# Kernel tuning notes

Hardware: AMD Instinct MI355X
Metric: run time of the kernel (lower is better)

## Reference

```python
import jax, jax.numpy as jnp
import numpy as np

FG_THR = 0.7
BG_THR = 0.3
NUM_PER_IMAGE = 256
NUM_POS_MAX = int(NUM_PER_IMAGE * 0.5)  # positive_ratio = 0.5
BBOX_W = (1.0, 1.0, 1.0, 1.0)
BETA = 1.0 / 9.0


def _permute(t, C):
    # N x (A*C) x H x W -> N x (H*W*A) x C, matching RPNLoss.permute
    N, _, H, W = t.shape
    t = t.reshape(N, -1, C, H, W)
    t = jnp.transpose(t, (0, 3, 4, 1, 2))
    return t.reshape(N, -1, C)


def _iou(a, b):
    # a: [N,4], b: [M,4] -> [N,M] (with +1 box convention, as in source)
    x_tl = jnp.maximum(a[:, None, 0], b[None, :, 0])
    y_tl = jnp.maximum(a[:, None, 1], b[None, :, 1])
    x_rb = jnp.minimum(a[:, None, 2], b[None, :, 2])
    y_rb = jnp.minimum(a[:, None, 3], b[None, :, 3])
    inter = jnp.clip(x_rb - x_tl + 1.0, 0.0) * jnp.clip(y_rb - y_tl + 1.0, 0.0)
    area1 = (a[:, 2] - a[:, 0] + 1.0) * (a[:, 3] - a[:, 1] + 1.0)
    area2 = (b[:, 2] - b[:, 0] + 1.0) * (b[:, 3] - b[:, 1] + 1.0)
    return inter / (area1[:, None] + area2[None, :] - inter)


def _encode(anchors, targets):
    ws = anchors[:, 2] - anchors[:, 0] + 1.0
    hs = anchors[:, 3] - anchors[:, 1] + 1.0
    x_ctr = anchors[:, 0] + 0.5 * ws
    y_ctr = anchors[:, 1] + 0.5 * hs
    t_ws = targets[:, 2] - targets[:, 0] + 1.0
    t_hs = targets[:, 3] - targets[:, 1] + 1.0
    t_x = targets[:, 0] + 0.5 * t_ws
    t_y = targets[:, 1] + 0.5 * t_hs
    wx, wy, ww, wh = BBOX_W
    tx = wx * (t_x - x_ctr) / ws
    ty = wy * (t_y - y_ctr) / hs
    tw = ww * jnp.log(t_ws / ws)
    th = wh * jnp.log(t_hs / hs)
    return jnp.stack([tx, ty, tw, th], axis=1)


def _bce_logits(l, t):
    return jnp.maximum(l, 0.0) - l * t + jnp.log1p(jnp.exp(-jnp.abs(l)))


def _per_image(anchor, logit, breg, size, target, key):
    N = anchor.shape[0]
    ious = _iou(anchor, target)  # [N, M]
    vals = ious.max(axis=1)
    ori = jnp.argmax(ious, axis=1).astype(jnp.int32)
    inds = jnp.where(vals < BG_THR, -1, ori)
    inds = jnp.where((vals >= BG_THR) & (vals < FG_THR), -2, inds)
    # low-quality matches: anchors achieving the per-target max IoU keep their argmax
    col_max = ious.max(axis=0)
    restore = (ious == col_max[None, :]).any(axis=1)
    inds = jnp.where(restore, ori, inds)
    # filter_anchors: keep anchors fully inside the image (size = (h, w))
    inside = (anchor[:, 0] >= 0) & (anchor[:, 1] >= 0) & \
             (anchor[:, 2] <= size[1] - 1.0) & (anchor[:, 3] <= size[0] - 1.0)
    inds = jnp.where(inside, inds, -2)

    pos = inds >= 0
    neg = inds == -1
    # random sampling via random priorities + fixed-size top_k with validity masks
    r = jax.random.uniform(key, (N,))
    pos_vals, pos_idx = jax.lax.top_k(jnp.where(pos, r, -1.0), NUM_POS_MAX)
    valid_pos = pos_vals >= 0.0
    num_pos = valid_pos.sum()
    neg_vals, neg_idx = jax.lax.top_k(jnp.where(neg, r, -1.0), NUM_PER_IMAGE)
    valid_neg = (neg_vals >= 0.0) & (jnp.arange(NUM_PER_IMAGE) < (NUM_PER_IMAGE - num_pos))

    # classification loss terms (BCE with logits); pos target 1, neg target 0
    vp = valid_pos.astype(logit.dtype)
    vn = valid_neg.astype(logit.dtype)
    cls_sum = jnp.sum(_bce_logits(logit[pos_idx], 1.0) * vp) + \
              jnp.sum(_bce_logits(logit[neg_idx], 0.0) * vn)
    count = num_pos + valid_neg.sum()

    m = jnp.clip(inds[pos_idx], 0, None)
    offsets = _encode(anchor[pos_idx], target[m])
    diff = jnp.abs(breg[pos_idx] - offsets)
    sl1 = jnp.where(diff < BETA, 0.5 * diff * diff / BETA, diff - 0.5 * BETA)
    reg_sum = jnp.sum(sl1 * vp[:, None])
    return cls_sum, count, reg_sum


def reference(anchors, logits, bbox_regs, sizes, targets):
    B = anchors.shape[0]
    log = _permute(logits, 1)[..., 0]      # [B, H*W*A]
    breg = _permute(bbox_regs, 4)          # [B, H*W*A, 4]
    keys = jax.random.split(jax.random.key(42), B)
    cls_s, cnt, reg_s = jax.vmap(_per_image)(anchors, log, breg, sizes, targets, keys)
    total = jnp.sum(cnt).astype(anchors.dtype)
    cls_loss = jnp.sum(cls_s) / total
    reg_loss = jnp.sum(reg_s) / total
    return jnp.stack([cls_loss, reg_loss])


def setup_inputs() -> dict:
    key = jax.random.key(0)
    ks = jax.random.split(key, 10)
    B, A, H, W, M = 4, 3, 168, 256, 32
    N = H * W * A
    IMG_H, IMG_W = 800.0, 1333.0
    x1 = jax.random.uniform(ks[0], (B, N)) * 1200.0
    y1 = jax.random.uniform(ks[1], (B, N)) * 700.0
    aw = jax.random.uniform(ks[2], (B, N)) * 300.0 + 16.0
    ah = jax.random.uniform(ks[3], (B, N)) * 300.0 + 16.0
    anchors = jnp.stack([x1, y1, x1 + aw, y1 + ah], axis=-1)  # some out of image -> filtered
    tx1 = jax.random.uniform(ks[4], (B, M)) * 1000.0
    ty1 = jax.random.uniform(ks[5], (B, M)) * 500.0
    tw = jax.random.uniform(ks[6], (B, M)) * 250.0 + 30.0
    th = jax.random.uniform(ks[7], (B, M)) * 200.0 + 30.0
    targets = jnp.stack([tx1, ty1, jnp.minimum(tx1 + tw, IMG_W - 1.0),
                         jnp.minimum(ty1 + th, IMG_H - 1.0)], axis=-1)
    logits = jax.random.normal(ks[8], (B, A, H, W), dtype=jnp.float32)
    bbox_regs = jax.random.normal(ks[9], (B, 4 * A, H, W), dtype=jnp.float32) * 0.1
    sizes = jnp.tile(jnp.array([IMG_H, IMG_W], dtype=jnp.float32), (B, 1))
    return {"anchors": anchors, "logits": logits, "bbox_regs": bbox_regs,
            "sizes": sizes, "targets": targets}
```

## Files before the change

### kernel.cpp

```cpp
#include <hip/hip_runtime.h>
#include <stdint.h>

#define Bn 4
#define An 3
#define Hn 168
#define Wn 256
#define Mn 32
#define HWn (Hn*Wn)
#define Nn (HWn*An)
#define POS_CAP 8192
#define NPERIM 256
#define NPOSMAX 128
#define FG_THR 0.7f
#define BG_THR 0.3f
#define BETA (1.0f/9.0f)

#define NBLK 126
#define APT 4
#define STRIDE (NBLK * 256)
#define NWAVES (NBLK * 4)
#define BUCKET_CAP 256
#define TSEG_CAP 256

#define OFF_POSCNT 0
#define OFF_COUNT  8
#define OFF_CLS    9
#define OFF_REG    10
#define OFF_DONE   11
#define OFF_BINCNT 16
#define OFF_BINBCE 4112
#define ZERO_WORDS 8208
#define OFF_WPCM   8208
#define OFF_TSEGC  72720
#define OFF_PLIST  74736
#define OFF_BUCKET 140272
#define OFF_TSEG   2237424

__device__ __forceinline__ uint32_t rotl32(uint32_t v, int n) { return (v << n) | (v >> (32 - n)); }

__device__ __forceinline__ void tf2x32(uint32_t k0, uint32_t k1, uint32_t x0, uint32_t x1,
                                       uint32_t& o0, uint32_t& o1) {
    uint32_t k2 = k0 ^ k1 ^ 0x1BD11BDAu;
    x0 += k0; x1 += k1;
    x0 += x1; x1 = rotl32(x1, 13); x1 ^= x0;
    x0 += x1; x1 = rotl32(x1, 15); x1 ^= x0;
    x0 += x1; x1 = rotl32(x1, 26); x1 ^= x0;
    x0 += x1; x1 = rotl32(x1, 6);  x1 ^= x0;
    x0 += k1; x1 += k2 + 1u;
    x0 += x1; x1 = rotl32(x1, 17); x1 ^= x0;
    x0 += x1; x1 = rotl32(x1, 29); x1 ^= x0;
    x0 += x1; x1 = rotl32(x1, 16); x1 ^= x0;
    x0 += x1; x1 = rotl32(x1, 24); x1 ^= x0;
    x0 += k2; x1 += k0 + 2u;
    x0 += x1; x1 = rotl32(x1, 13); x1 ^= x0;
    x0 += x1; x1 = rotl32(x1, 15); x1 ^= x0;
    x0 += x1; x1 = rotl32(x1, 26); x1 ^= x0;
    x0 += x1; x1 = rotl32(x1, 6);  x1 ^= x0;
    x0 += k0; x1 += k1 + 3u;
    x0 += x1; x1 = rotl32(x1, 17); x1 ^= x0;
    x0 += x1; x1 = rotl32(x1, 29); x1 ^= x0;
    x0 += x1; x1 = rotl32(x1, 16); x1 ^= x0;
    x0 += x1; x1 = rotl32(x1, 24); x1 ^= x0;
    x0 += k1; x1 += k2 + 4u;
    x0 += x1; x1 = rotl32(x1, 13); x1 ^= x0;
    x0 += x1; x1 = rotl32(x1, 15); x1 ^= x0;
    x0 += x1; x1 = rotl32(x1, 26); x1 ^= x0;
    x0 += x1; x1 = rotl32(x1, 6);  x1 ^= x0;
    x0 += k2; x1 += k0 + 5u;
    o0 = x0; o1 = x1;
}

__device__ __forceinline__ uint32_t rng_m23(uint32_t k0, uint32_t k1, uint32_t i) {
    uint32_t o0, o1;
    tf2x32(k0, k1, 0u, i, o0, o1);
    return (o0 ^ o1) >> 9;
}

__device__ __forceinline__ uint32_t vload(const uint32_t* p) {
    return *(const volatile uint32_t*)p;
}

__device__ __forceinline__ float iou_one(float a0, float a1, float a2, float a3,
                                         float t0, float t1, float t2, float t3) {
    float xtl = fmaxf(a0, t0), ytl = fmaxf(a1, t1);
    float xrb = fminf(a2, t2), yrb = fminf(a3, t3);
    float iw = fmaxf(xrb - xtl + 1.0f, 0.0f);
    float ih = fmaxf(yrb - ytl + 1.0f, 0.0f);
    float inter = iw * ih;
    float area1 = (a2 - a0 + 1.0f) * (a3 - a1 + 1.0f);
    float area2 = (t2 - t0 + 1.0f) * (t3 - t1 + 1.0f);
    return inter * __builtin_amdgcn_rcpf(area1 + area2 - inter);
}

__device__ __forceinline__ float bce0(float l) {
    return fmaxf(l, 0.0f) + log1pf(expf(-fabsf(l)));
}

__device__ __forceinline__ bool sel_less(uint2 a, uint2 b) {
    return (a.x > b.x) || (a.x == b.x && a.y < b.y);
}

__device__ void bitonic_sort_shared(uint2* buf, int n) {
    for (int k = 2; k <= n; k <<= 1) {
        for (int j = k >> 1; j > 0; j >>= 1) {
            for (int t = (int)threadIdx.x; t < n; t += (int)blockDim.x) {
                int ixj = t ^ j;
                if (ixj > t) {
                    uint2 x = buf[t], y = buf[ixj];
                    bool up = ((t & k) == 0);
                    bool sw = up ? sel_less(y, x) : sel_less(x, y);
                    if (sw) { buf[t] = y; buf[ixj] = x; }
                }
            }
            __syncthreads();
        }
    }
}

__global__ void __launch_bounds__(256) k0_init(uint32_t* __restrict__ ws) {
    int i = blockIdx.x * 256 + (int)threadIdx.x;
    if (i < ZERO_WORDS) ws[i] = 0u;
}

__global__ void __launch_bounds__(256) k1_iou(const float* __restrict__ anchors,
                                              const float* __restrict__ targets,
                                              const float* __restrict__ sizes,
                                              const float* __restrict__ logits,
                                              uint32_t* __restrict__ ws) {
    const int b = blockIdx.y, j = blockIdx.x, tid = threadIdx.x;
    const int wid = tid >> 6, lane = tid & 63;

    uint32_t key0, key1;
    tf2x32(0u, 42u, 0u, (uint32_t)b, key0, key1);

    const int base = j * 256 + tid;
    float4 av[APT];
    #pragma unroll
    for (int k = 0; k < APT; ++k)
        av[k] = ((const float4*)anchors)[b * Nn + base + k * STRIDE];

    float rowmax[APT]; int ori[APT]; uint32_t tie[APT];
    #pragma unroll
    for (int k = 0; k < APT; ++k) { rowmax[k] = -1.0f; ori[k] = 0; tie[k] = 0u; }

    float mycm = 0.0f;
    #pragma unroll 4
    for (int t = 0; t < Mn; ++t) {
        float4 tv = ((const float4*)targets)[b * Mn + t];
        float io[APT];
        float m0 = 0.0f;
        #pragma unroll
        for (int k = 0; k < APT; ++k) {
            io[k] = iou_one(av[k].x, av[k].y, av[k].z, av[k].w, tv.x, tv.y, tv.z, tv.w);
            if (io[k] > rowmax[k]) { rowmax[k] = io[k]; ori[k] = t; }
            m0 = fmaxf(m0, io[k]);
        }
        #pragma unroll
        for (int o = 32; o > 0; o >>= 1) m0 = fmaxf(m0, __shfl_xor(m0, o, 64));
        if (lane == t) mycm = m0;
        #pragma unroll
        for (int k = 0; k < APT; ++k)
            tie[k] |= (io[k] == m0) ? (1u << t) : 0u;
    }

    const int wimg = j * 4 + wid;
    if (lane < Mn)
        ws[OFF_WPCM + ((size_t)b * NWAVES + wimg) * 32 + lane] = __float_as_uint(mycm);

    const float sh = sizes[b * 2 + 0], sw = sizes[b * 2 + 1];
    unsigned long long lt_mask = (lane == 63) ? 0x7FFFFFFFFFFFFFFFull
                                              : ((1ull << lane) - 1ull);
    uint4* tseg = (uint4*)(ws + OFF_TSEG) + ((size_t)b * NWAVES + wimg) * TSEG_CAP;
    uint32_t wcnt = 0;
    #pragma unroll
    for (int k = 0; k < APT; ++k) {
        const int i = base + k * STRIDE;
        bool inside = (av[k].x >= 0.0f) && (av[k].y >= 0.0f) &&
                      (av[k].z <= sw - 1.0f) && (av[k].w <= sh - 1.0f);
        bool fg = rowmax[k] >= FG_THR;
        bool bg = rowmax[k] < BG_THR;
        bool posn   = inside && fg;
        bool defern = inside && !fg && (tie[k] != 0u);
        bool negn   = inside && bg && (tie[k] == 0u);
        uint32_t m = rng_m23(key0, key1, (uint32_t)i);

        unsigned long long pmask = __ballot(posn);
        if (pmask) {
            int leader = __ffsll((long long)pmask) - 1;
            uint32_t bb = 0;
            if (lane == leader) bb = atomicAdd(&ws[OFF_POSCNT + b], (uint32_t)__popcll(pmask));
            bb = __shfl(bb, leader, 64);
            if (posn) {
                uint32_t p = bb + (uint32_t)__popcll(pmask & lt_mask);
                if (p < POS_CAP)
                    ((uint2*)(ws + OFF_PLIST))[(size_t)b * POS_CAP + p] =
                        make_uint2(m, (uint32_t)i | ((uint32_t)ori[k] << 17));
            }
        }
        unsigned long long dmask = __ballot(defern);
        if (defern) {
            uint32_t slot = wcnt + (uint32_t)__popcll(dmask & lt_mask);
            tseg[slot] = make_uint4(tie[k], m,
                                    (uint32_t)i | ((uint32_t)ori[k] << 17) | (bg ? (1u << 22) : 0u),
                                    0u);
        }
        wcnt += (uint32_t)__popcll(dmask);
        if (negn) {
            int bin = (int)(m >> 13);
            uint32_t slot = atomicAdd(&ws[OFF_BINCNT + (b << 10) + bin], 1u);
            if (slot < BUCKET_CAP)
                ((uint2*)(ws + OFF_BUCKET))[((((size_t)b << 10) + bin) << 8) + slot] =
                    make_uint2(m, (uint32_t)i);
            int a = i % An, hw = i / An;
            float l = logits[(b * An + a) * HWn + hw];
            atomicAdd((float*)&ws[OFF_BINBCE + (b << 10) + bin], bce0(l));
        }
    }
    if (lane == 0) ws[OFF_TSEGC + b * NWAVES + wimg] = wcnt;
}

__global__ void __launch_bounds__(1024) k3_final(const float* __restrict__ anchors,
                                                 const float* __restrict__ targets,
                                                 const float* __restrict__ logits,
                                                 const float* __restrict__ bregs,
                                                 uint32_t* __restrict__ ws,
                                                 float* __restrict__ out) {
    const int b = blockIdx.x, tid = threadIdx.x;
    __shared__ uint32_t cmbits[Mn];
    __shared__ float fred[1024];
    __shared__ uint32_t eq[512];
    __shared__ uint32_t incl[512];
    __shared__ uint32_t csum[1024];
    __shared__ uint2 buf[2048];
    __shared__ int s_bd, s_need;
    float cls = 0.0f, reg = 0.0f;

    {
        int t = tid & 31, sub = tid >> 5;
        float acc = 0.0f;
        for (int w = sub; w < NWAVES; w += 32)
            acc = fmaxf(acc, __uint_as_float(ws[OFF_WPCM + ((size_t)b * NWAVES + w) * 32 + t]));
        fred[tid] = acc;
        __syncthreads();
        if (sub == 0) {
            #pragma unroll
            for (int q = 1; q < 32; ++q) acc = fmaxf(acc, fred[t + 32 * q]);
            cmbits[t] = __float_as_uint(acc);
        }
    }
    __syncthreads();

    if (tid < NWAVES) {
        const uint32_t* wp = ws + OFF_WPCM + ((size_t)b * NWAVES + tid) * 32;
        uint32_t e = 0;
        #pragma unroll 8
        for (int t2 = 0; t2 < Mn; ++t2)
            e |= (wp[t2] == cmbits[t2]) ? (1u << t2) : 0u;
        eq[tid] = e;
    }
    if (tid < 512) incl[tid] = (tid < NWAVES) ? ws[OFF_TSEGC + b * NWAVES + tid] : 0u;
    __syncthreads();
    for (int off = 1; off < 512; off <<= 1) {
        uint32_t v = 0;
        if (tid < 512) { v = incl[tid]; if (tid >= off) v += incl[tid - off]; }
        __syncthreads();
        if (tid < 512) incl[tid] = v;
        __syncthreads();
    }
    const int ttotal = (int)incl[511];

    for (int f = tid; f < ttotal; f += 1024) {
        int lo = 0, hi = 511;
        while (lo < hi) { int mid = (lo + hi) >> 1; if ((int)incl[mid] > f) hi = mid; else lo = mid + 1; }
        const int w = lo;
        const int o = f - ((w > 0) ? (int)incl[w - 1] : 0);
        uint4 e = ((const uint4*)(ws + OFF_TSEG))[((size_t)b * NWAVES + w) * TSEG_CAP + o];
        int i = (int)(e.z & 0x1FFFFu);
        if (e.x & eq[w]) {
            uint32_t p = atomicAdd(&ws[OFF_POSCNT + b], 1u);
            if (p < POS_CAP)
                ((uint2*)(ws + OFF_PLIST))[(size_t)b * POS_CAP + p] =
                    make_uint2(e.y, e.z & 0x3FFFFFu);
        } else if (e.z & (1u << 22)) {
            uint32_t m = e.y;
            int bin = (int)(m >> 13);
            uint32_t slot = atomicAdd(&ws[OFF_BINCNT + (b << 10) + bin], 1u);
            if (slot < BUCKET_CAP)
                ((uint2*)(ws + OFF_BUCKET))[((((size_t)b << 10) + bin) << 8) + slot] =
                    make_uint2(m, (uint32_t)i);
            int a = i % An, hw = i / An;
            float l = logits[(b * An + a) * HWn + hw];
            atomicAdd((float*)&ws[OFF_BINBCE + (b << 10) + bin], bce0(l));
        }
    }
    __syncthreads();

    csum[tid] = vload(ws + OFF_BINCNT + (b << 10) + tid);
    __syncthreads();
    for (int off = 1; off < 1024; off <<= 1) {
        uint32_t v = csum[tid];
        uint32_t add = (tid + off < 1024) ? csum[tid + off] : 0u;
        __syncthreads();
        csum[tid] = v + add;
        __syncthreads();
    }
    uint32_t pc = vload(ws + OFF_POSCNT + b);
    int num_pos = (pc < (uint32_t)NPOSMAX) ? (int)pc : NPOSMAX;
    int k_neg = NPERIM - num_pos;
    uint32_t total = csum[0];
    if (tid == 0 && (int)total < k_neg) { s_bd = -1; s_need = 0; }
    {
        uint32_t inclv = csum[tid];
        uint32_t nxt = (tid < 1023) ? csum[tid + 1] : 0u;
        if ((int)total >= k_neg && (int)inclv >= k_neg && (int)nxt < k_neg) {
            s_bd = tid; s_need = k_neg - (int)nxt;
        }
    }
    if (tid == 0) {
        int sel_negs = ((int)total < k_neg) ? (int)total : k_neg;
        atomicAdd(&ws[OFF_COUNT], (uint32_t)(num_pos + sel_negs));
    }
    __syncthreads();
    const int bd = s_bd, need = s_need;
    if ((int)tid > bd)
        cls += __uint_as_float(vload(ws + OFF_BINBCE + (b << 10) + tid));
    __syncthreads();

    if (need > 0) {
        int cnt = (int)vload(ws + OFF_BINCNT + (b << 10) + bd);
        if (cnt > BUCKET_CAP) cnt = BUCKET_CAP;
        const uint2* bkt = (const uint2*)(ws + OFF_BUCKET) + ((((size_t)b << 10) + bd) << 8);
        for (int t = tid; t < cnt; t += 1024) buf[t] = bkt[t];
        int npad = 1; while (npad < cnt) npad <<= 1;
        for (int t = tid; t < npad; t += 1024) if (t >= cnt) buf[t] = make_uint2(0u, 0xFFFFFFFFu);
        __syncthreads();
        bitonic_sort_shared(buf, npad);
        int sel = (need < cnt) ? need : cnt;
        for (int t = tid; t < sel; t += 1024) {
            int i = (int)buf[t].y;
            int a = i % An, hw = i / An;
            float l = logits[(b * An + a) * HWn + hw];
            cls += bce0(l);
        }
    }
    __syncthreads();

    {
        int pci = (pc < (uint32_t)POS_CAP) ? (int)pc : POS_CAP;
        const uint2* plist = (const uint2*)(ws + OFF_PLIST) + (size_t)b * POS_CAP;
        int psel = (pci < NPOSMAX) ? pci : NPOSMAX;
        bool use_buf = false;
        if (pci > NPOSMAX) {
            int n = (pci < 2048) ? pci : 2048;
            for (int t = tid; t < n; t += 1024) buf[t] = plist[t];
            int npad = 1; while (npad < n) npad <<= 1;
            for (int t = tid; t < npad; t += 1024) if (t >= n) buf[t] = make_uint2(0u, 0xFFFFFFFFu);
            __syncthreads();
            bitonic_sort_shared(buf, npad);
            use_buf = true;
            psel = (NPOSMAX < n) ? NPOSMAX : n;
        }
        for (int t = tid; t < psel; t += 1024) {
            uint32_t packed = use_buf ? buf[t].y : plist[t].y;
            int i = (int)(packed & 0x1FFFFu);
            int orit = (int)((packed >> 17) & 0x1Fu);
            int a = i % An, hw = i / An;
            float l = logits[(b * An + a) * HWn + hw];
            cls += fmaxf(l, 0.0f) - l + log1pf(expf(-fabsf(l)));
            float4 avx = ((const float4*)anchors)[b * Nn + i];
            float4 tv = ((const float4*)targets)[b * Mn + orit];
            float aws = avx.z - avx.x + 1.0f, ahs = avx.w - avx.y + 1.0f;
            float axc = avx.x + 0.5f * aws, ayc = avx.y + 0.5f * ahs;
            float tws = tv.z - tv.x + 1.0f, ths = tv.w - tv.y + 1.0f;
            float txc = tv.x + 0.5f * tws, tyc = tv.y + 0.5f * ths;
            float off0 = (txc - axc) / aws;
            float off1 = (tyc - ayc) / ahs;
            float off2 = logf(tws / aws);
            float off3 = logf(ths / ahs);
            float br0 = bregs[(b * 12 + a * 4 + 0) * HWn + hw];
            float br1 = bregs[(b * 12 + a * 4 + 1) * HWn + hw];
            float br2 = bregs[(b * 12 + a * 4 + 2) * HWn + hw];
            float br3 = bregs[(b * 12 + a * 4 + 3) * HWn + hw];
            float d;
            d = fabsf(br0 - off0); reg += (d < BETA) ? 0.5f * d * d / BETA : d - 0.5f * BETA;
            d = fabsf(br1 - off1); reg += (d < BETA) ? 0.5f * d * d / BETA : d - 0.5f * BETA;
            d = fabsf(br2 - off2); reg += (d < BETA) ? 0.5f * d * d / BETA : d - 0.5f * BETA;
            d = fabsf(br3 - off3); reg += (d < BETA) ? 0.5f * d * d / BETA : d - 0.5f * BETA;
        }
    }

    fred[tid] = cls;
    __syncthreads();
    for (int s = 512; s > 0; s >>= 1) {
        if (tid < s) fred[tid] += fred[tid + s];
        __syncthreads();
    }
    if (tid == 0 && fred[0] != 0.0f) atomicAdd((float*)&ws[OFF_CLS], fred[0]);
    __syncthreads();
    fred[tid] = reg;
    __syncthreads();
    for (int s = 512; s > 0; s >>= 1) {
        if (tid < s) fred[tid] += fred[tid + s];
        __syncthreads();
    }
    if (tid == 0) {
        if (fred[0] != 0.0f) atomicAdd((float*)&ws[OFF_REG], fred[0]);
        __threadfence();
        uint32_t old = atomicAdd(&ws[OFF_DONE], 1u);
        if (old == Bn - 1) {
            float cls_tot = __uint_as_float(atomicAdd(&ws[OFF_CLS], 0u));
            float reg_tot = __uint_as_float(atomicAdd(&ws[OFF_REG], 0u));
            float cnt = (float)atomicAdd(&ws[OFF_COUNT], 0u);
            out[0] = cls_tot / cnt;
            out[1] = reg_tot / cnt;
        }
    }
}

extern "C" void kernel_launch(void* const* d_in, const int* in_sizes, int n_in,
                              void* d_out, int out_size, void* d_ws, size_t ws_size,
                              hipStream_t stream) {
    const float* anchors = (const float*)d_in[0];
    const float* logits  = (const float*)d_in[1];
    const float* bregs   = (const float*)d_in[2];
    const float* sizes   = (const float*)d_in[3];
    const float* targets = (const float*)d_in[4];
    float* out = (float*)d_out;
    uint32_t* ws = (uint32_t*)d_ws;

    k0_init<<<dim3((ZERO_WORDS + 255) / 256), dim3(256), 0, stream>>>(ws);
    k1_iou<<<dim3(NBLK, Bn), dim3(256), 0, stream>>>(anchors, targets, sizes, logits, ws);
    k3_final<<<dim3(Bn), dim3(1024), 0, stream>>>(anchors, targets, logits, bregs, ws, out);
}
```

Measured before the change: 181.4 us.

## Move deferred-anchor resolution from single-block final kernel into parallel resolve kernel

Resolving deferred anchors (the low-quality-match restore check and negative bucketing) moves out of the 4-block k3_final into a new k2_resolve kernel launched over NBLK x B blocks. Each k1 block now also writes a per-block column-max partial, so k2 only reduces 126 entries instead of 504. Position-list appends are aggregated per wave with ballot plus a single atomicAdd. This spreads a serial tail across the whole GPU, at the cost of an extra kernel launch and some redundant per-block column-max reduction.

```diff
diff --git a/kernel.cpp b/kernel.cpp
--- a/kernel.cpp
+++ b/kernel.cpp
@@ -30,11 +30,12 @@
 #define OFF_BINCNT 16
 #define OFF_BINBCE 4112
 #define ZERO_WORDS 8208
-#define OFF_WPCM   8208
-#define OFF_TSEGC  72720
-#define OFF_PLIST  74736
-#define OFF_BUCKET 140272
-#define OFF_TSEG   2237424
+#define OFF_PCM    8208
+#define OFF_WPCM   24336
+#define OFF_TSEGC  88848
+#define OFF_PLIST  90864
+#define OFF_BUCKET 156400
+#define OFF_TSEG   2253552
 
 __device__ __forceinline__ uint32_t rotl32(uint32_t v, int n) { return (v << n) | (v >> (32 - n)); }
 
@@ -129,6 +130,7 @@
                                               uint32_t* __restrict__ ws) {
     const int b = blockIdx.y, j = blockIdx.x, tid = threadIdx.x;
     const int wid = tid >> 6, lane = tid & 63;
+    __shared__ float part[4][Mn];
 
     uint32_t key0, key1;
     tf2x32(0u, 42u, 0u, (uint32_t)b, key0, key1);
@@ -164,8 +166,16 @@
     }
 
     const int wimg = j * 4 + wid;
-    if (lane < Mn)
+    if (lane < Mn) {
         ws[OFF_WPCM + ((size_t)b * NWAVES + wimg) * 32 + lane] = __float_as_uint(mycm);
+        part[wid][lane] = mycm;
+    }
+    __syncthreads();
+    if (tid < Mn) {
+        float v = fmaxf(fmaxf(part[0][tid], part[1][tid]),
+                        fmaxf(part[2][tid], part[3][tid]));
+        ws[OFF_PCM + ((size_t)b * NBLK + j) * Mn + tid] = __float_as_uint(v);
+    }
 
     const float sh = sizes[b * 2 + 0], sw = sizes[b * 2 + 1];
     unsigned long long lt_mask = (lane == 63) ? 0x7FFFFFFFFFFFFFFFull
@@ -219,69 +229,69 @@
     if (lane == 0) ws[OFF_TSEGC + b * NWAVES + wimg] = wcnt;
 }
 
-__global__ void __launch_bounds__(1024) k3_final(const float* __restrict__ anchors,
-                                                 const float* __restrict__ targets,
-                                                 const float* __restrict__ logits,
-                                                 const float* __restrict__ bregs,
-                                                 uint32_t* __restrict__ ws,
-                                                 float* __restrict__ out) {
-    const int b = blockIdx.x, tid = threadIdx.x;
-    __shared__ uint32_t cmbits[Mn];
-    __shared__ float fred[1024];
-    __shared__ uint32_t eq[512];
-    __shared__ uint32_t incl[512];
-    __shared__ uint32_t csum[1024];
-    __shared__ uint2 buf[2048];
-    __shared__ int s_bd, s_need;
-    float cls = 0.0f, reg = 0.0f;
+__global__ void __launch_bounds__(256) k2_resolve(const float* __restrict__ logits,
+                                                  uint32_t* __restrict__ ws) {
+    const int b = blockIdx.y, j = blockIdx.x, tid = threadIdx.x;
+    const int lane = tid & 63;
+    __shared__ float redf[256];
+    __shared__ uint32_t cmb[Mn];
+    __shared__ uint32_t eqs[4];
+    __shared__ uint32_t cnts[4];
 
     {
         int t = tid & 31, sub = tid >> 5;
         float acc = 0.0f;
-        for (int w = sub; w < NWAVES; w += 32)
-            acc = fmaxf(acc, __uint_as_float(ws[OFF_WPCM + ((size_t)b * NWAVES + w) * 32 + t]));
-        fred[tid] = acc;
+        for (int jj = sub; jj < NBLK; jj += 8)
+            acc = fmaxf(acc, __uint_as_float(ws[OFF_PCM + ((size_t)b * NBLK + jj) * Mn + t]));
+        redf[tid] = acc;
         __syncthreads();
         if (sub == 0) {
             #pragma unroll
-            for (int q = 1; q < 32; ++q) acc = fmaxf(acc, fred[t + 32 * q]);
-            cmbits[t] = __float_as_uint(acc);
-        }
-    }
-    __syncthreads();
-
-    if (tid < NWAVES) {
-        const uint32_t* wp = ws + OFF_WPCM + ((size_t)b * NWAVES + tid) * 32;
-        uint32_t e = 0;
-        #pragma unroll 8
-        for (int t2 = 0; t2 < Mn; ++t2)
-            e |= (wp[t2] == cmbits[t2]) ? (1u << t2) : 0u;
-        eq[tid] = e;
-    }
-    if (tid < 512) incl[tid] = (tid < NWAVES) ? ws[OFF_TSEGC + b * NWAVES + tid] : 0u;
-    __syncthreads();
-    for (int off = 1; off < 512; off <<= 1) {
-        uint32_t v = 0;
-        if (tid < 512) { v = incl[tid]; if (tid >= off) v += incl[tid - off]; }
-        __syncthreads();
-        if (tid < 512) incl[tid] = v;
-        __syncthreads();
-    }
-    const int ttotal = (int)incl[511];
-
-    for (int f = tid; f < ttotal; f += 1024) {
-        int lo = 0, hi = 511;
-        while (lo < hi) { int mid = (lo + hi) >> 1; if ((int)incl[mid] > f) hi = mid; else lo = mid + 1; }
-        const int w = lo;
-        const int o = f - ((w > 0) ? (int)incl[w - 1] : 0);
-        uint4 e = ((const uint4*)(ws + OFF_TSEG))[((size_t)b * NWAVES + w) * TSEG_CAP + o];
+            for (int q = 1; q < 8; ++q) acc = fmaxf(acc, redf[t + 32 * q]);
+            cmb[t] = __float_as_uint(acc);
+        }
+    }
+    if (tid < 4) {
+        eqs[tid] = 0u;
+        cnts[tid] = ws[OFF_TSEGC + b * NWAVES + j * 4 + tid];
+    }
+    __syncthreads();
+    if (tid < 128) {
+        int lw = tid >> 5, t2 = tid & 31;
+        uint32_t wv = ws[OFF_WPCM + ((size_t)b * NWAVES + j * 4 + lw) * 32 + t2];
+        if (wv == cmb[t2]) atomicOr(&eqs[lw], 1u << t2);
+    }
+    __syncthreads();
+
+    const uint32_t c0 = cnts[0], c1 = cnts[1], c2 = cnts[2], c3 = cnts[3];
+    const int total = (int)(c0 + c1 + c2 + c3);
+    unsigned long long lt_mask = (lane == 63) ? 0x7FFFFFFFFFFFFFFFull
+                                              : ((1ull << lane) - 1ull);
+    for (int f = tid; f < total; f += 256) {
+        int lw, o;
+        if ((uint32_t)f < c0)                { lw = 0; o = f; }
+        else if ((uint32_t)f < c0 + c1)      { lw = 1; o = f - (int)c0; }
+        else if ((uint32_t)f < c0 + c1 + c2) { lw = 2; o = f - (int)(c0 + c1); }
+        else                                 { lw = 3; o = f - (int)(c0 + c1 + c2); }
+        uint4 e = ((const uint4*)(ws + OFF_TSEG))
+                      [((size_t)b * NWAVES + j * 4 + lw) * TSEG_CAP + o];
         int i = (int)(e.z & 0x1FFFFu);
-        if (e.x & eq[w]) {
-            uint32_t p = atomicAdd(&ws[OFF_POSCNT + b], 1u);
-            if (p < POS_CAP)
-                ((uint2*)(ws + OFF_PLIST))[(size_t)b * POS_CAP + p] =
-                    make_uint2(e.y, e.z & 0x3FFFFFu);
-        } else if (e.z & (1u << 22)) {
+        bool restored = (e.x & eqs[lw]) != 0u;
+
+        unsigned long long rmask = __ballot(restored);
+        if (rmask) {
+            int leader = __ffsll((long long)rmask) - 1;
+            uint32_t bb = 0;
+            if (lane == leader) bb = atomicAdd(&ws[OFF_POSCNT + b], (uint32_t)__popcll(rmask));
+            bb = __shfl(bb, leader, 64);
+            if (restored) {
+                uint32_t p = bb + (uint32_t)__popcll(rmask & lt_mask);
+                if (p < POS_CAP)
+                    ((uint2*)(ws + OFF_PLIST))[(size_t)b * POS_CAP + p] =
+                        make_uint2(e.y, e.z & 0x3FFFFFu);
+            }
+        }
+        if (!restored && (e.z & (1u << 22))) {
             uint32_t m = e.y;
             int bin = (int)(m >> 13);
             uint32_t slot = atomicAdd(&ws[OFF_BINCNT + (b << 10) + bin], 1u);
@@ -293,7 +303,20 @@
             atomicAdd((float*)&ws[OFF_BINBCE + (b << 10) + bin], bce0(l));
         }
     }
-    __syncthreads();
+}
+
+__global__ void __launch_bounds__(1024) k3_final(const float* __restrict__ anchors,
+                                                 const float* __restrict__ targets,
+                                                 const float* __restrict__ logits,
+                                                 const float* __restrict__ bregs,
+                                                 uint32_t* __restrict__ ws,
+                                                 float* __restrict__ out) {
+    const int b = blockIdx.x, tid = threadIdx.x;
+    __shared__ uint32_t csum[1024];
+    __shared__ uint2 buf[2048];
+    __shared__ float fred[1024];
+    __shared__ int s_bd, s_need;
+    float cls = 0.0f, reg = 0.0f;
 
     csum[tid] = vload(ws + OFF_BINCNT + (b << 10) + tid);
     __syncthreads();
@@ -430,5 +453,6 @@
 
     k0_init<<<dim3((ZERO_WORDS + 255) / 256), dim3(256), 0, stream>>>(ws);
     k1_iou<<<dim3(NBLK, Bn), dim3(256), 0, stream>>>(anchors, targets, sizes, logits, ws);
+    k2_resolve<<<dim3(NBLK, Bn), dim3(256), 0, stream>>>(logits, ws);
     k3_final<<<dim3(Bn), dim3(1024), 0, stream>>>(anchors, targets, logits, bregs, ws, out);
 }
```

After: 154.6 us. -14.8%, faster.
